# Kernel optimization log

Measured on AMD Instinct MI355X. Metric: run time of the kernel, lower is better.

The kernel has to match this reference:

```python
import jax, jax.numpy as jnp
import numpy as np
import math

N_HEADS = 16

def _layernorm(x, g, b):
    m = x.mean(-1, keepdims=True)
    v = ((x - m) ** 2).mean(-1, keepdims=True)
    return (x - m) * jax.lax.rsqrt(v + 1e-5) * g + b

def _project(x):
    # Poincare ball (c=1) projection: clip last-dim norm to 1 - eps
    max_norm = 1.0 - 1e-5
    n = jnp.linalg.norm(x, axis=-1, keepdims=True)
    return jnp.where(n > max_norm, x * (max_norm / jnp.maximum(n, 1e-12)), x)


def setup_inputs() -> dict:
    key = jax.random.key(0)
    ks = jax.random.split(key, 8)
    B, L, D = 2, 2048, 1024
    w = lambda k, s: jax.random.normal(k, s, jnp.float32) * 0.02
    return dict(
        x=jax.random.normal(ks[0], (B, L, D), jnp.float32),
        wq=w(ks[1], (D, D)), bq=jnp.zeros((D,), jnp.float32),
        wk=w(ks[2], (D, D)), bk=jnp.zeros((D,), jnp.float32),
        wv=w(ks[3], (D, D)), bv=jnp.zeros((D,), jnp.float32),
        wo=w(ks[4], (D, D)), bo=jnp.zeros((D,), jnp.float32),
        g1=jnp.ones((D,), jnp.float32), b1=jnp.zeros((D,), jnp.float32),
        g2=jnp.ones((D,), jnp.float32), b2=jnp.zeros((D,), jnp.float32),
        w1=w(ks[5], (4 * D, D)), bf1=jnp.zeros((4 * D,), jnp.float32),
        w2=w(ks[6], (D, 4 * D)), bf2=jnp.zeros((D,), jnp.float32),
    )


def reference(x, wq, bq, wk, bk, wv, bv, wo, bo, g1, b1, g2, b2, w1, bf1, w2, bf2):
    B, L, D = x.shape
    H = N_HEADS
    hd = D // H
    temp = math.sqrt(hd)

    xn = _layernorm(x, g1, b1)

    def heads(w, b):
        y = xn @ w.T + b                       # [B, L, D]
        return y.reshape(B, L, H, hd).transpose(0, 2, 1, 3)  # [B, H, L, hd]

    q = _project(heads(wq, bq))
    k = _project(heads(wk, bk))
    v = heads(wv, bv)

    # -||q - k||^2 / temp, via ||q||^2 + ||k||^2 - 2 q.k (same math as the
    # explicit broadcast-diff in the torch code, expressed as a GEMM)
    q2 = (q ** 2).sum(-1)[..., :, None]        # [B, H, L, 1]
    k2 = (k ** 2).sum(-1)[..., None, :]        # [B, H, 1, L]
    qk = jnp.einsum('bhld,bhmd->bhlm', q, k)   # [B, H, L, L]
    scores = -(q2 + k2 - 2.0 * qk) / temp
    attn = jax.nn.softmax(scores, axis=-1)     # dropout = identity (eval mode)

    out = jnp.einsum('bhlm,bhmd->bhld', attn, v)
    out = out.transpose(0, 2, 1, 3).reshape(B, L, D) @ wo.T + bo

    x = _project(x + out)
    xn2 = _layernorm(x, g2, b2)
    h = jax.nn.gelu(xn2 @ w1.T + bf1, approximate=False)  # torch nn.GELU = erf
    x = _project(x + (h @ w2.T + bf2))
    return x
```

## Files before the change

kernel.cpp:

```cpp
#include <hip/hip_runtime.h>
#include <math.h>

#define SEQ_L 2048
#define DM    1024
#define NH    16
#define HD    64
#define BL    4096
#define DFF   4096
#define QKV_S 3072

typedef __attribute__((ext_vector_type(8))) short short8;
typedef __attribute__((ext_vector_type(4))) short s16x4;
typedef __attribute__((ext_vector_type(4))) float f32x4;

__device__ __forceinline__ short f2bf(float x) {
    unsigned u = __float_as_uint(x);
    u += 0x7fff + ((u >> 16) & 1);
    return (short)(u >> 16);
}
__device__ __forceinline__ float bf2f(short s) {
    return __uint_as_float(((unsigned)(unsigned short)s) << 16);
}

__device__ __forceinline__ float gelu_fast(float x) {
    const float xa = fabsf(x);
    const float z = xa * 0.70710678118654752440f;
    const float t = __builtin_amdgcn_rcpf(fmaf(0.3275911f, z, 1.f));
    float P = fmaf(t, 1.061405429f, -1.453152027f);
    P = fmaf(t, P, 1.421413741f);
    P = fmaf(t, P, -0.284496736f);
    P = fmaf(t, P, 0.254829592f);
    P *= t;
    const float e = __expf(-z * z);
    const float erfp = fmaf(-P, e, 1.f);
    return 0.5f * fmaf(xa, erfp, x);
}

__device__ __forceinline__ float block_sum(float v, float* red, int tid) {
#pragma unroll
    for (int m = 32; m; m >>= 1) v += __shfl_xor(v, m);
    if ((tid & 63) == 0) red[tid >> 6] = v;
    __syncthreads();
    v = red[0] + red[1] + red[2] + red[3];
    __syncthreads();
    return v;
}

__global__ __launch_bounds__(256) void cvt6_kernel(
    const float* __restrict__ wq, const float* __restrict__ wk,
    const float* __restrict__ wv, const float* __restrict__ wo,
    const float* __restrict__ w1, const float* __restrict__ w2,
    short* __restrict__ dst) {
    const size_t i = (size_t)blockIdx.x * 256 + threadIdx.x;
    const float* src;
    size_t off;
    if (i < 1048576) {
        const int seg = (int)(i >> 18);
        off = i & 262143;
        src = seg == 0 ? wq : seg == 1 ? wk : seg == 2 ? wv : wo;
    } else if (i < 2097152) { src = w1; off = i - 1048576; }
    else                    { src = w2; off = i - 2097152; }
    const float4 v = ((const float4*)src)[off];
    const s16x4 o = {f2bf(v.x), f2bf(v.y), f2bf(v.z), f2bf(v.w)};
    ((s16x4*)dst)[i] = o;
}

__global__ __launch_bounds__(256) void ln_bf16_kernel(const float* __restrict__ x,
                                                      const float* __restrict__ g,
                                                      const float* __restrict__ b,
                                                      short* __restrict__ out) {
    const int row = blockIdx.x;
    const int tid = threadIdx.x;
    __shared__ float red[4];
    const float4 xv = *(const float4*)(x + (size_t)row * DM + tid * 4);
    float s = xv.x + xv.y + xv.z + xv.w;
    s = block_sum(s, red, tid);
    const float mean = s * (1.f / (float)DM);
    float dx0 = xv.x - mean, dx1 = xv.y - mean, dx2 = xv.z - mean, dx3 = xv.w - mean;
    float ss = dx0 * dx0 + dx1 * dx1 + dx2 * dx2 + dx3 * dx3;
    ss = block_sum(ss, red, tid);
    const float rs = 1.f / sqrtf(ss * (1.f / (float)DM) + 1e-5f);
    const float4 gv = *(const float4*)(g + tid * 4);
    const float4 bv = *(const float4*)(b + tid * 4);
    const s16x4 ob = {f2bf(dx0 * rs * gv.x + bv.x), f2bf(dx1 * rs * gv.y + bv.y),
                      f2bf(dx2 * rs * gv.z + bv.z), f2bf(dx3 * rs * gv.w + bv.w)};
    *(s16x4*)(out + (size_t)row * DM + tid * 4) = ob;
}

__global__ __launch_bounds__(256) void resproj_kernel(const float* __restrict__ a,
                                                      const float* __restrict__ c,
                                                      float* __restrict__ out) {
    const int row = blockIdx.x;
    const int tid = threadIdx.x;
    __shared__ float red[4];
    const float4 av = *(const float4*)(a + (size_t)row * DM + tid * 4);
    const float4 cv = *(const float4*)(c + (size_t)row * DM + tid * 4);
    float4 sv;
    sv.x = av.x + cv.x; sv.y = av.y + cv.y; sv.z = av.z + cv.z; sv.w = av.w + cv.w;
    float ss = sv.x * sv.x + sv.y * sv.y + sv.z * sv.z + sv.w * sv.w;
    ss = block_sum(ss, red, tid);
    const float n = sqrtf(ss);
    const float mx = 1.f - 1e-5f;
    const float scale = (n > mx) ? (mx / fmaxf(n, 1e-12f)) : 1.f;
    sv.x *= scale; sv.y *= scale; sv.z *= scale; sv.w *= scale;
    *(float4*)(out + (size_t)row * DM + tid * 4) = sv;
}

__global__ __launch_bounds__(256) void qk_prep(const short* __restrict__ qkvB,
                                               short* __restrict__ Qb,
                                               short* __restrict__ Kb,
                                               float* __restrict__ k2) {
    const int tid = threadIdx.x, lane = tid & 63;
    const int vec = blockIdx.x * 4 + (tid >> 6);
    const int row = vec >> 4, h = vec & 15;
    const int b = row >> 11, l = row & 2047;
    const size_t dstv = ((size_t)(b * NH + h) * SEQ_L + l) * HD + lane;
    const float mx = 1.f - 1e-5f;
    {
        const float v = bf2f(qkvB[(size_t)row * QKV_S + h * HD + lane]);
        float s = v * v;
#pragma unroll
        for (int m = 32; m; m >>= 1) s += __shfl_xor(s, m);
        const float n = sqrtf(s);
        const float sc = (n > mx) ? (mx / fmaxf(n, 1e-12f)) : 1.f;
        Qb[dstv] = f2bf(v * sc);
    }
    {
        const float v = bf2f(qkvB[(size_t)row * QKV_S + DM + h * HD + lane]);
        float s = v * v;
#pragma unroll
        for (int m = 32; m; m >>= 1) s += __shfl_xor(s, m);
        const float n = sqrtf(s);
        const float sc = (n > mx) ? (mx / fmaxf(n, 1e-12f)) : 1.f;
        Kb[dstv] = f2bf(v * sc);
        if (lane == 0) k2[(size_t)(b * NH + h) * SEQ_L + l] = s * sc * sc * 0.125f;
    }
}

__global__ __launch_bounds__(256) void v_prep(const short* __restrict__ qkvB,
                                              short* __restrict__ Vtb) {
    const int blk = blockIdx.x;
    const int bh = blk >> 5, kt = blk & 31;
    const int b = bh >> 4, h = bh & 15;
    __shared__ short T[64 * 72];
    const int tid = threadIdx.x;
    {
        const int key = tid >> 2, ch = (tid & 3) * 16;
        const size_t src = ((size_t)b * SEQ_L + kt * 64 + key) * QKV_S + 2 * DM + h * HD + ch;
        *(short8*)&T[key * 72 + ch]     = *(const short8*)(qkvB + src);
        *(short8*)&T[key * 72 + ch + 8] = *(const short8*)(qkvB + src + 8);
    }
    __syncthreads();
    const int hd = tid >> 2, kc = (tid & 3) * 16;
    short8 o0, o1;
#pragma unroll
    for (int j = 0; j < 8; ++j) {
        o0[j] = T[(kc + j) * 72 + hd];
        o1[j] = T[(kc + 8 + j) * 72 + hd];
    }
    short* dst = Vtb + ((size_t)bh * HD + hd) * SEQ_L + kt * 64 + kc;
    *(short8*)dst = o0;
    *(short8*)(dst + 8) = o1;
}

template <int BM, int ACT, int OUTBF, int FUSED>
__global__ __launch_bounds__(256) void gemm_mfma(
    const short* __restrict__ A, const short* __restrict__ Bw,
    const float* __restrict__ bb0, const float* __restrict__ bb1,
    const float* __restrict__ bb2, void* __restrict__ Cout,
    int M, int N, int K) {
    constexpr int RT = BM / 32;
    constexpr bool VEPI = (OUTBF != 0) && (BM == 128);
    constexpr int SMEM_BYTES = VEPI ? (4 * 64 * 72 * 2) : ((BM * 32 + 128 * 32) * 2);
    __shared__ __align__(16) char raw[SMEM_BYTES];
    short* As = (short*)raw;
    short* Bs = As + BM * 32;
    const int tid = threadIdx.x;
    const int wv = tid >> 6, lane = tid & 63;
    const int m0 = blockIdx.y * BM, n0 = blockIdx.x * 128;
    const int wr = (wv & 1) * (BM / 2);
    const int wc = (wv >> 1) * 64;

    const int arow = wv * (BM / 4) + (lane >> 2);
    const int brow = wv * 32 + (lane >> 2);
    const short* Ag = A + (size_t)(m0 + arow) * K + (lane & 3) * 8;
    const short* Bg = Bw + (size_t)(n0 + brow) * K + (lane & 3) * 8;
    short* AsW = As + (wv * (BM / 4)) * 32 + lane * 8;
    short* AsW2 = AsW + 16 * 32;
    short* BsW = Bs + (wv * 32) * 32 + lane * 8;
    short* BsW2 = BsW + 16 * 32;

    const f32x4 z4 = {0.f, 0.f, 0.f, 0.f};
    f32x4 acc[RT][4];
#pragma unroll
    for (int r = 0; r < RT; ++r)
#pragma unroll
        for (int c = 0; c < 4; ++c) acc[r][c] = z4;

    const int lrow = lane & 15, kq = (lane >> 4) * 8;

    short8 ra0, ra1, rb0, rb1;
    ra0 = *(const short8*)(Ag);
    if constexpr (BM == 128) ra1 = *(const short8*)(Ag + (size_t)16 * K);
    rb0 = *(const short8*)(Bg);
    rb1 = *(const short8*)(Bg + (size_t)16 * K);

    for (int kt = 0; kt < K; kt += 32) {
        __syncthreads();
        *(short8*)AsW = ra0;
        if constexpr (BM == 128) *(short8*)AsW2 = ra1;
        *(short8*)BsW = rb0;
        *(short8*)BsW2 = rb1;
        short8 na0, na1, nb0, nb1;
        if (kt + 32 < K) {
            na0 = *(const short8*)(Ag + kt + 32);
            if constexpr (BM == 128) na1 = *(const short8*)(Ag + (size_t)16 * K + kt + 32);
            nb0 = *(const short8*)(Bg + kt + 32);
            nb1 = *(const short8*)(Bg + (size_t)16 * K + kt + 32);
        }
        __syncthreads();
        short8 af[RT], bf[4];
#pragma unroll
        for (int r = 0; r < RT; ++r)
            af[r] = *(const short8*)&As[(wr + r * 16 + lrow) * 32 + kq];
#pragma unroll
        for (int c = 0; c < 4; ++c)
            bf[c] = *(const short8*)&Bs[(wc + c * 16 + lrow) * 32 + kq];
#pragma unroll
        for (int r = 0; r < RT; ++r)
#pragma unroll
            for (int c = 0; c < 4; ++c)
                acc[r][c] = __builtin_amdgcn_mfma_f32_16x16x32_bf16(af[r], bf[c], acc[r][c], 0, 0, 0);
        ra0 = na0; ra1 = na1; rb0 = nb0; rb1 = nb1;
    }

    const int col = lane & 15, rb = (lane >> 4) * 4;
    if constexpr (VEPI) {
        __syncthreads();
        short* Ot = (short*)raw + wv * (64 * 72);
#pragma unroll
        for (int c = 0; c < 4; ++c) {
            const int gn = n0 + wc + c * 16 + col;
            float bias;
            if constexpr (FUSED) {
                const int seg = gn >> 10;
                bias = (seg == 0 ? bb0 : seg == 1 ? bb1 : bb2)[gn & 1023];
            } else {
                bias = bb0[gn];
            }
#pragma unroll
            for (int r = 0; r < RT; ++r)
#pragma unroll
                for (int i = 0; i < 4; ++i) {
                    float v = acc[r][c][i] + bias;
                    if constexpr (ACT) v = gelu_fast(v);
                    Ot[(r * 16 + rb + i) * 72 + c * 16 + col] = f2bf(v);
                }
        }
        const int orow = lane >> 3, oc = (lane & 7) * 8;
#pragma unroll
        for (int it = 0; it < 8; ++it) {
            const short8 vv = *(const short8*)&Ot[(it * 8 + orow) * 72 + oc];
            *(short8*)((short*)Cout + (size_t)(m0 + wr + it * 8 + orow) * N + n0 + wc + oc) = vv;
        }
    } else {
#pragma unroll
        for (int c = 0; c < 4; ++c) {
            const int gn = n0 + wc + c * 16 + col;
            float bias;
            if constexpr (FUSED) {
                const int seg = gn >> 10;
                bias = (seg == 0 ? bb0 : seg == 1 ? bb1 : bb2)[gn & 1023];
            } else {
                bias = bb0[gn];
            }
#pragma unroll
            for (int r = 0; r < RT; ++r) {
                const int gm = m0 + wr + r * 16 + rb;
#pragma unroll
                for (int i = 0; i < 4; ++i) {
                    float v = acc[r][c][i] + bias;
                    if constexpr (ACT) v = gelu_fast(v);
                    if constexpr (OUTBF)
                        ((short*)Cout)[(size_t)(gm + i) * N + gn] = f2bf(v);
                    else
                        ((float*)Cout)[(size_t)(gm + i) * N + gn] = v;
                }
            }
        }
    }
}

__global__ __launch_bounds__(256) void attn_mfma2(const short* __restrict__ Qb,
                                                  const short* __restrict__ Kb,
                                                  const short* __restrict__ Vtb,
                                                  const float* __restrict__ k2v,
                                                  short* __restrict__ aO) {
    const int qt = blockIdx.x, h = blockIdx.y, b = blockIdx.z;
    const int tid = threadIdx.x, wv = tid >> 6, lane = tid & 63;
    const int bh = b * NH + h;
    __shared__ __align__(16) short smem[2 * 64 * 72];
    short* Ks = smem;
    short* Vt = smem + 64 * 72;
    const int lrow = lane & 15, q8 = (lane >> 4) * 8, q4 = (lane >> 4) * 4;

    const short* Qh = Qb + (size_t)bh * SEQ_L * HD;
    const short* Kh = Kb + (size_t)bh * SEQ_L * HD;
    const short* Vh = Vtb + (size_t)bh * HD * SEQ_L;
    const float* k2p = k2v + (size_t)bh * SEQ_L;

    short8 qf[2][2];
#pragma unroll
    for (int nt = 0; nt < 2; ++nt)
#pragma unroll
        for (int kc = 0; kc < 2; ++kc)
            qf[nt][kc] = *(const short8*)(Qh +
                (size_t)(qt * 128 + wv * 32 + nt * 16 + lrow) * HD + kc * 32 + q8);

    const f32x4 z4 = {0.f, 0.f, 0.f, 0.f};
    f32x4 o[4][2];
#pragma unroll
    for (int ht = 0; ht < 4; ++ht)
#pragma unroll
        for (int nt = 0; nt < 2; ++nt) o[ht][nt] = z4;
    float lsum[2] = {0.f, 0.f};

    const int srow = tid >> 2, sch = (tid & 3) * 16;

    for (int kt = 0; kt < SEQ_L / 64; ++kt) {
        const int k0 = kt * 64;
        __syncthreads();
        {
            const short* g = Kh + (size_t)(k0 + srow) * HD + sch;
            *(short8*)&Ks[srow * 72 + sch]     = *(const short8*)g;
            *(short8*)&Ks[srow * 72 + sch + 8] = *(const short8*)(g + 8);
            const short* gv = Vh + (size_t)srow * SEQ_L + k0 + sch;
            *(short8*)&Vt[srow * 72 + sch]     = *(const short8*)gv;
            *(short8*)&Vt[srow * 72 + sch + 8] = *(const short8*)(gv + 8);
        }
        __syncthreads();

        short8 p8[2][2];
#pragma unroll
        for (int mt = 0; mt < 4; ++mt) {
            const short8 kf0 = *(const short8*)&Ks[(mt * 16 + lrow) * 72 + q8];
            const short8 kf1 = *(const short8*)&Ks[(mt * 16 + lrow) * 72 + 32 + q8];
            const float4 kk = *(const float4*)(k2p + k0 + mt * 16 + q4);
            const int c = mt >> 1, hi = (mt & 1) * 4;
#pragma unroll
            for (int nt = 0; nt < 2; ++nt) {
                f32x4 s = z4;
                s = __builtin_amdgcn_mfma_f32_16x16x32_bf16(kf0, qf[nt][0], s, 0, 0, 0);
                s = __builtin_amdgcn_mfma_f32_16x16x32_bf16(kf1, qf[nt][1], s, 0, 0, 0);
#pragma unroll
                for (int i = 0; i < 4; ++i) {
                    const float kki = (i == 0) ? kk.x : (i == 1) ? kk.y : (i == 2) ? kk.z : kk.w;
                    const float p = __expf(fmaf(s[i], 0.25f, -kki));
                    lsum[nt] += p;
                    p8[nt][c][hi + i] = f2bf(p);
                }
            }
        }
#pragma unroll
        for (int ht = 0; ht < 4; ++ht) {
#pragma unroll
            for (int c = 0; c < 2; ++c) {
                const s16x4 va = *(const s16x4*)&Vt[(ht * 16 + lrow) * 72 + c * 32 + q4];
                const s16x4 vb = *(const s16x4*)&Vt[(ht * 16 + lrow) * 72 + c * 32 + 16 + q4];
                const short8 v8 = {va[0], va[1], va[2], va[3], vb[0], vb[1], vb[2], vb[3]};
#pragma unroll
                for (int nt = 0; nt < 2; ++nt)
                    o[ht][nt] = __builtin_amdgcn_mfma_f32_16x16x32_bf16(v8, p8[nt][c], o[ht][nt], 0, 0, 0);
            }
        }
    }

#pragma unroll
    for (int nt = 0; nt < 2; ++nt) {
        lsum[nt] += __shfl_xor(lsum[nt], 16);
        lsum[nt] += __shfl_xor(lsum[nt], 32);
    }
    const float inv0 = 1.f / lsum[0], inv1 = 1.f / lsum[1];

    __syncthreads();
    short* Ot = smem + wv * (32 * 72);
#pragma unroll
    for (int ht = 0; ht < 4; ++ht)
#pragma unroll
        for (int nt = 0; nt < 2; ++nt) {
            const float iv = nt ? inv1 : inv0;
            const s16x4 ov = {f2bf(o[ht][nt][0] * iv), f2bf(o[ht][nt][1] * iv),
                              f2bf(o[ht][nt][2] * iv), f2bf(o[ht][nt][3] * iv)};
            *(s16x4*)&Ot[(nt * 16 + lrow) * 72 + ht * 16 + q4] = ov;
        }
    const int erow = lane >> 1, ec = (lane & 1) * 32;
    const short8 r0 = *(const short8*)&Ot[erow * 72 + ec + 0];
    const short8 r1 = *(const short8*)&Ot[erow * 72 + ec + 8];
    const short8 r2 = *(const short8*)&Ot[erow * 72 + ec + 16];
    const short8 r3 = *(const short8*)&Ot[erow * 72 + ec + 24];
    short* dst = aO + ((size_t)b * SEQ_L + qt * 128 + wv * 32 + erow) * DM + h * HD + ec;
    *(short8*)(dst + 0)  = r0;
    *(short8*)(dst + 8)  = r1;
    *(short8*)(dst + 16) = r2;
    *(short8*)(dst + 24) = r3;
}

extern "C" void kernel_launch(void* const* d_in, const int* in_sizes, int n_in,
                              void* d_out, int out_size, void* d_ws, size_t ws_size,
                              hipStream_t stream) {
    const float* x   = (const float*)d_in[0];
    const float* wq  = (const float*)d_in[1];
    const float* bq  = (const float*)d_in[2];
    const float* wk  = (const float*)d_in[3];
    const float* bk  = (const float*)d_in[4];
    const float* wv  = (const float*)d_in[5];
    const float* bv  = (const float*)d_in[6];
    const float* wo  = (const float*)d_in[7];
    const float* bo  = (const float*)d_in[8];
    const float* g1  = (const float*)d_in[9];
    const float* b1  = (const float*)d_in[10];
    const float* g2  = (const float*)d_in[11];
    const float* b2  = (const float*)d_in[12];
    const float* w1  = (const float*)d_in[13];
    const float* bf1 = (const float*)d_in[14];
    const float* w2  = (const float*)d_in[15];
    const float* bf2 = (const float*)d_in[16];
    float* out = (float*)d_out;

    char* base = (char*)d_ws;
    short* wbf  = (short*)base;
    short* qkvB = (short*)(base + (24u << 20));
    short* xnb  = (short*)(base + (48u << 20));
    short* Qb   = xnb;
    short* Kb   = (short*)(base + (56u << 20));
    short* Vtb  = (short*)(base + (64u << 20));
    float* k2   = (float*)(base + (72u << 20));
    short* aO   = (short*)(base + (72u << 20) + (256u << 10));
    float* P    = (float*)(base + (24u << 20));
    short* xn2b = Vtb;
    short* hbuf = qkvB;
    float* y2   = (float*)(base + (58u << 20));

    cvt6_kernel<<<12288, 256, 0, stream>>>(wq, wk, wv, wo, w1, w2, wbf);
    ln_bf16_kernel<<<BL, 256, 0, stream>>>(x, g1, b1, xnb);
    gemm_mfma<128, 0, 1, 1><<<dim3(24, 32), 256, 0, stream>>>(
        xnb, wbf, bq, bk, bv, qkvB, BL, QKV_S, DM);
    qk_prep<<<16384, 256, 0, stream>>>(qkvB, Qb, Kb, k2);
    v_prep<<<1024, 256, 0, stream>>>(qkvB, Vtb);
    attn_mfma2<<<dim3(16, 16, 2), 256, 0, stream>>>(Qb, Kb, Vtb, k2, aO);
    gemm_mfma<64, 0, 0, 0><<<dim3(8, 64), 256, 0, stream>>>(
        aO, wbf + 3145728, bo, bo, bo, P, BL, DM, DM);
    resproj_kernel<<<BL, 256, 0, stream>>>(x, P, out);
    ln_bf16_kernel<<<BL, 256, 0, stream>>>(out, g2, b2, xn2b);
    gemm_mfma<128, 1, 1, 0><<<dim3(32, 32), 256, 0, stream>>>(
        xn2b, wbf + 4194304, bf1, bf1, bf1, hbuf, BL, DFF, DM);
    gemm_mfma<64, 0, 0, 0><<<dim3(8, 64), 256, 0, stream>>>(
        hbuf, wbf + 8388608, bf2, bf2, bf2, y2, BL, DM, DFF);
    resproj_kernel<<<BL, 256, 0, stream>>>(out, y2, out);
}
```

Baseline: 399.1 us.

## Split-K the two N=1024 projection GEMMs and sum partials in residual kernel

The output-projection and FFN down-projection GEMMs now launch with a second grid dimension that splits K in half. Each half writes its own fp32 partial buffer, and the residual+projection kernel adds both partials. The aim is more workgroups for these 512-block launches so the GPU's compute units are better filled. In exchange it writes an extra fp32 partial buffer and reads it back in the residual kernel. Workspace offsets must stay clear of live buffers: Ya aliases the bf16 weight region start, which at that point still holds the Q/K/V weights rather than the w2 weights being read.

```diff
diff --git a/kernel.cpp b/kernel.cpp
--- a/kernel.cpp
+++ b/kernel.cpp
@@ -87,16 +87,21 @@
     *(s16x4*)(out + (size_t)row * DM + tid * 4) = ob;
 }
 
-__global__ __launch_bounds__(256) void resproj_kernel(const float* __restrict__ a,
-                                                      const float* __restrict__ c,
-                                                      float* __restrict__ out) {
+__global__ __launch_bounds__(256) void resproj3_kernel(const float* __restrict__ a,
+                                                       const float* __restrict__ c0,
+                                                       const float* __restrict__ c1,
+                                                       float* __restrict__ out) {
     const int row = blockIdx.x;
     const int tid = threadIdx.x;
     __shared__ float red[4];
     const float4 av = *(const float4*)(a + (size_t)row * DM + tid * 4);
-    const float4 cv = *(const float4*)(c + (size_t)row * DM + tid * 4);
+    const float4 c0v = *(const float4*)(c0 + (size_t)row * DM + tid * 4);
+    const float4 c1v = *(const float4*)(c1 + (size_t)row * DM + tid * 4);
     float4 sv;
-    sv.x = av.x + cv.x; sv.y = av.y + cv.y; sv.z = av.z + cv.z; sv.w = av.w + cv.w;
+    sv.x = av.x + c0v.x + c1v.x;
+    sv.y = av.y + c0v.y + c1v.y;
+    sv.z = av.z + c0v.z + c1v.z;
+    sv.w = av.w + c0v.w + c1v.w;
     float ss = sv.x * sv.x + sv.y * sv.y + sv.z * sv.z + sv.w * sv.w;
     ss = block_sum(ss, red, tid);
     const float n = sqrtf(ss);
@@ -168,7 +173,7 @@
     const short* __restrict__ A, const short* __restrict__ Bw,
     const float* __restrict__ bb0, const float* __restrict__ bb1,
     const float* __restrict__ bb2, void* __restrict__ Cout,
-    int M, int N, int K) {
+    void* __restrict__ Cout1, int M, int N, int K, int Kst) {
     constexpr int RT = BM / 32;
     constexpr bool VEPI = (OUTBF != 0) && (BM == 128);
     constexpr int SMEM_BYTES = VEPI ? (4 * 64 * 72 * 2) : ((BM * 32 + 128 * 32) * 2);
@@ -178,13 +183,15 @@
     const int tid = threadIdx.x;
     const int wv = tid >> 6, lane = tid & 63;
     const int m0 = blockIdx.y * BM, n0 = blockIdx.x * 128;
+    const int zz = blockIdx.z;
+    const int koff = zz * K;
     const int wr = (wv & 1) * (BM / 2);
     const int wc = (wv >> 1) * 64;
 
     const int arow = wv * (BM / 4) + (lane >> 2);
     const int brow = wv * 32 + (lane >> 2);
-    const short* Ag = A + (size_t)(m0 + arow) * K + (lane & 3) * 8;
-    const short* Bg = Bw + (size_t)(n0 + brow) * K + (lane & 3) * 8;
+    const short* Ag = A + (size_t)(m0 + arow) * Kst + koff + (lane & 3) * 8;
+    const short* Bg = Bw + (size_t)(n0 + brow) * Kst + koff + (lane & 3) * 8;
     short* AsW = As + (wv * (BM / 4)) * 32 + lane * 8;
     short* AsW2 = AsW + 16 * 32;
     short* BsW = Bs + (wv * 32) * 32 + lane * 8;
@@ -201,9 +208,9 @@
 
     short8 ra0, ra1, rb0, rb1;
     ra0 = *(const short8*)(Ag);
-    if constexpr (BM == 128) ra1 = *(const short8*)(Ag + (size_t)16 * K);
+    if constexpr (BM == 128) ra1 = *(const short8*)(Ag + (size_t)16 * Kst);
     rb0 = *(const short8*)(Bg);
-    rb1 = *(const short8*)(Bg + (size_t)16 * K);
+    rb1 = *(const short8*)(Bg + (size_t)16 * Kst);
 
     for (int kt = 0; kt < K; kt += 32) {
         __syncthreads();
@@ -214,9 +221,9 @@
         short8 na0, na1, nb0, nb1;
         if (kt + 32 < K) {
             na0 = *(const short8*)(Ag + kt + 32);
-            if constexpr (BM == 128) na1 = *(const short8*)(Ag + (size_t)16 * K + kt + 32);
+            if constexpr (BM == 128) na1 = *(const short8*)(Ag + (size_t)16 * Kst + kt + 32);
             nb0 = *(const short8*)(Bg + kt + 32);
-            nb1 = *(const short8*)(Bg + (size_t)16 * K + kt + 32);
+            nb1 = *(const short8*)(Bg + (size_t)16 * Kst + kt + 32);
         }
         __syncthreads();
         short8 af[RT], bf[4];
@@ -264,6 +271,7 @@
             *(short8*)((short*)Cout + (size_t)(m0 + wr + it * 8 + orow) * N + n0 + wc + oc) = vv;
         }
     } else {
+        float* outp = (float*)(zz ? Cout1 : Cout);
 #pragma unroll
         for (int c = 0; c < 4; ++c) {
             const int gn = n0 + wc + c * 16 + col;
@@ -274,6 +282,7 @@
             } else {
                 bias = bb0[gn];
             }
+            if (zz) bias = 0.f;
 #pragma unroll
             for (int r = 0; r < RT; ++r) {
                 const int gm = m0 + wr + r * 16 + rb;
@@ -282,9 +291,9 @@
                     float v = acc[r][c][i] + bias;
                     if constexpr (ACT) v = gelu_fast(v);
                     if constexpr (OUTBF)
-                        ((short*)Cout)[(size_t)(gm + i) * N + gn] = f2bf(v);
+                        ((short*)outp)[(size_t)(gm + i) * N + gn] = f2bf(v);
                     else
-                        ((float*)Cout)[(size_t)(gm + i) * N + gn] = v;
+                        outp[(size_t)(gm + i) * N + gn] = v;
                 }
             }
         }
@@ -436,25 +445,27 @@
     short* Vtb  = (short*)(base + (64u << 20));
     float* k2   = (float*)(base + (72u << 20));
     short* aO   = (short*)(base + (72u << 20) + (256u << 10));
-    float* P    = (float*)(base + (24u << 20));
+    float* Pa   = (float*)(base + (24u << 20));
+    float* Pb   = (float*)(base + (41u << 20));
     short* xn2b = Vtb;
     short* hbuf = qkvB;
-    float* y2   = (float*)(base + (58u << 20));
+    float* Ya   = (float*)base;
+    float* Yb   = (float*)(base + (58u << 20));
 
     cvt6_kernel<<<12288, 256, 0, stream>>>(wq, wk, wv, wo, w1, w2, wbf);
     ln_bf16_kernel<<<BL, 256, 0, stream>>>(x, g1, b1, xnb);
     gemm_mfma<128, 0, 1, 1><<<dim3(24, 32), 256, 0, stream>>>(
-        xnb, wbf, bq, bk, bv, qkvB, BL, QKV_S, DM);
+        xnb, wbf, bq, bk, bv, qkvB, nullptr, BL, QKV_S, DM, DM);
     qk_prep<<<16384, 256, 0, stream>>>(qkvB, Qb, Kb, k2);
     v_prep<<<1024, 256, 0, stream>>>(qkvB, Vtb);
     attn_mfma2<<<dim3(16, 16, 2), 256, 0, stream>>>(Qb, Kb, Vtb, k2, aO);
-    gemm_mfma<64, 0, 0, 0><<<dim3(8, 64), 256, 0, stream>>>(
-        aO, wbf + 3145728, bo, bo, bo, P, BL, DM, DM);
-    resproj_kernel<<<BL, 256, 0, stream>>>(x, P, out);
+    gemm_mfma<64, 0, 0, 0><<<dim3(8, 64, 2), 256, 0, stream>>>(
+        aO, wbf + 3145728, bo, bo, bo, Pa, Pb, BL, DM, DM / 2, DM);
+    resproj3_kernel<<<BL, 256, 0, stream>>>(x, Pa, Pb, out);
     ln_bf16_kernel<<<BL, 256, 0, stream>>>(out, g2, b2, xn2b);
     gemm_mfma<128, 1, 1, 0><<<dim3(32, 32), 256, 0, stream>>>(
-        xn2b, wbf + 4194304, bf1, bf1, bf1, hbuf, BL, DFF, DM);
-    gemm_mfma<64, 0, 0, 0><<<dim3(8, 64), 256, 0, stream>>>(
-        hbuf, wbf + 8388608, bf2, bf2, bf2, y2, BL, DM, DFF);
-    resproj_kernel<<<BL, 256, 0, stream>>>(out, y2, out);
-}
+        xn2b, wbf + 4194304, bf1, bf1, bf1, hbuf, nullptr, BL, DFF, DM, DM);
+    gemm_mfma<64, 0, 0, 0><<<dim3(8, 64, 2), 256, 0, stream>>>(
+        hbuf, wbf + 8388608, bf2, bf2, bf2, Ya, Yb, BL, DM, DFF / 2, DFF);
+    resproj3_kernel<<<BL, 256, 0, stream>>>(out, Ya, Yb, out);
+}
```

Result: slower. 407.8 us (+2.2%).
